# Optimization experiments

Hardware: AMD Instinct MI355X
Metric: run time of the kernel (lower is better)

Reference implementation:

```python
import jax, jax.numpy as jnp
import numpy as np

B, T, D, H, O = 256, 512, 128, 256, 128

def setup_inputs() -> dict:
    key = jax.random.key(0)
    ks = jax.random.split(key, 7)
    s = lambda k, shape, fan: jax.random.normal(k, shape, dtype=jnp.float32) / np.sqrt(fan)
    return {
        "x": jax.random.normal(ks[0], (B, T, D), dtype=jnp.float32),
        "W_hx_w": s(ks[1], (H, D), D),
        "W_hx_b": jnp.zeros((H,), jnp.float32),
        "W_hh_w": s(ks[2], (H, H), H),
        "W_hh_b": jnp.zeros((H,), jnp.float32),
        "W_ph_w": s(ks[3], (O, H), H),
        "W_ph_b": jnp.zeros((O,), jnp.float32),
    }

def reference(x, W_hx_w, W_hx_b, W_hh_w, W_hh_b, W_ph_w, W_ph_b):
    # Precompute the input projection for all timesteps in one batched GEMM.
    xW = jnp.einsum('btd,hd->bth', x, W_hx_w) + W_hx_b  # [B,T,H]
    h0 = jnp.zeros((x.shape[0], W_hh_w.shape[0]), x.dtype)

    def step(h, xw_t):
        h_new = jnp.tanh(xw_t + h @ W_hh_w.T + W_hh_b)
        return h_new, None

    h_T, _ = jax.lax.scan(step, h0, jnp.swapaxes(xW, 0, 1))  # scan over T
    out = h_T @ W_ph_w.T + W_ph_b  # [B,O]
    return out
```

## Files before the change

### kernel.cpp

```cpp
#include <hip/hip_runtime.h>


typedef _Float16 f16;
typedef _Float16 f16x2 __attribute__((ext_vector_type(2)));
typedef _Float16 f16x4 __attribute__((ext_vector_type(4)));
typedef _Float16 f16x8 __attribute__((ext_vector_type(8)));
typedef float f32x4 __attribute__((ext_vector_type(4)));

#define NB 256
#define NT 512
#define ND 128
#define NH 256
#define NO 128
#define R  16
#define TCH 8
#define NCH (NT / TCH)
#define STEP_F16 4096
#define WS_NEED ((size_t)16 * NT * STEP_F16 * 2)

__device__ __forceinline__ float fast_tanh(float z) {
  float e = __builtin_amdgcn_exp2f(z * 2.88539008177793f);
  float r = __builtin_amdgcn_rcpf(e + 1.0f);
  return __builtin_fmaf(-2.0f, r, 1.0f);
}

__device__ __forceinline__ f16x8 cvt8(const float* __restrict__ p) {
  f32x4 v0 = *(const f32x4*)p;
  f32x4 v1 = *(const f32x4*)(p + 4);
  f16x8 r;
  r[0] = (f16)v0.x; r[1] = (f16)v0.y; r[2] = (f16)v0.z; r[3] = (f16)v0.w;
  r[4] = (f16)v1.x; r[5] = (f16)v1.y; r[6] = (f16)v1.z; r[7] = (f16)v1.w;
  return r;
}

__global__ __launch_bounds__(256, 1)
void xw_gemm(const float* __restrict__ x,
             const float* __restrict__ Wx, const float* __restrict__ bx,
             const float* __restrict__ bh, f16* __restrict__ ws)
{
  const int wgb = blockIdx.x & 15;
  const int c   = blockIdx.x >> 4;
  const int tid = threadIdx.x;
  const int w   = tid >> 6;
  const int l15 = tid & 15;
  const int g   = (tid >> 4) & 3;

  __shared__ alignas(16) f16 xlds[TCH * R][ND];

  f16x8 fWx[4][4];
  f32x4 bias4[4];
  #pragma unroll
  for (int ct = 0; ct < 4; ++ct) {
    const int j = w * 64 + ct * 16 + l15;
    #pragma unroll
    for (int kt = 0; kt < 4; ++kt)
      fWx[ct][kt] = cvt8(Wx + (size_t)j * ND + kt * 32 + g * 8);
    const int j0 = w * 64 + ct * 16 + g * 4;
    #pragma unroll
    for (int rg = 0; rg < 4; ++rg)
      bias4[ct][rg] = bx[j0 + rg] + bh[j0 + rg];
  }

  const int srow = tid >> 4;
  const int sq   = tid & 15;
  const float* xc = x + ((size_t)(wgb * R + srow) * NT + (size_t)c * TCH) * ND;
  #pragma unroll
  for (int jj = 0; jj < 16; ++jj) {
    const int f = (sq + jj * 16) * 4;
    f32x4 v = *(const f32x4*)(xc + f);
    const int t = f >> 7;
    const int d = f & (ND - 1);
    const int m = t * R + srow;
    f16x4 h4;
    h4[0] = (f16)v.x; h4[1] = (f16)v.y; h4[2] = (f16)v.z; h4[3] = (f16)v.w;
    *(f16x4*)((char*)&xlds[m][0] + ((2 * d) ^ ((m & 7) << 4))) = h4;
  }
  __syncthreads();

  #pragma unroll
  for (int t = 0; t < TCH; ++t) {
    f16x8 b[4];
    #pragma unroll
    for (int kt = 0; kt < 4; ++kt) {
      const int m = t * R + l15;
      b[kt] = *(const f16x8*)((char*)&xlds[m][0] +
               ((kt * 64 + g * 16) ^ ((m & 7) << 4)));
    }
    f16* wsp = ws + ((size_t)(wgb * NT + c * TCH + t)) * STEP_F16
                  + w * 1024 + g * 64 + l15 * 4;
    #pragma unroll
    for (int ct = 0; ct < 4; ++ct) {
      f32x4 ac = bias4[ct];
      #pragma unroll
      for (int kt = 0; kt < 4; ++kt)
        ac = __builtin_amdgcn_mfma_f32_16x16x32_f16(fWx[ct][kt], b[kt], ac, 0, 0, 0);
      f16x4 p;
      p[0] = (f16)ac[0]; p[1] = (f16)ac[1]; p[2] = (f16)ac[2]; p[3] = (f16)ac[3];
      *(f16x4*)(wsp + ct * 256) = p;
    }
  }
}

#define DO_STEP(CUR, ACIN, ACOUT, XWPF, XWIN, TAU)                          \
  {                                                                         \
    f16x8 bfr[8];                                                           \
    _Pragma("unroll")                                                       \
    for (int kt = 0; kt < 8; ++kt)                                          \
      bfr[kt] = *(const f16x8*)((const char*)&hbuf[CUR][l15][0] +           \
                ((kt * 64 + g * 16) ^ ((l15 & 7) << 4)));                   \
    int pf = (TAU) + 2; pf = pf < NT ? pf : NT - 1;                         \
    _Pragma("unroll")                                                       \
    for (int ct = 0; ct < 2; ++ct)                                          \
      XWPF[ct] = *(const f16x4*)(wsg + (size_t)pf * STEP_F16 + ct * 256);   \
    _Pragma("unroll")                                                       \
    for (int ct = 0; ct < 2; ++ct) {                                        \
      _Pragma("unroll")                                                     \
      for (int kt = 0; kt < 8; ++kt)                                        \
        ACIN[ct] = __builtin_amdgcn_mfma_f32_16x16x32_f16(fWh[ct][kt],      \
                     bfr[kt], ACIN[ct], 0, 0, 0);                           \
    }                                                                       \
    _Pragma("unroll")                                                       \
    for (int ct = 0; ct < 2; ++ct) {                                        \
      f16x4 h4;                                                             \
      _Pragma("unroll")                                                     \
      for (int rg = 0; rg < 4; ++rg)                                        \
        h4[rg] = (f16)fast_tanh(ACIN[ct][rg]);                              \
      *(f16x4*)((char*)&hbuf[(CUR) ^ 1][l15][0] +                           \
                ((64 * w2 + 32 * ct + 8 * g) ^ ((l15 & 7) << 4))) = h4;     \
    }                                                                       \
    _Pragma("unroll")                                                       \
    for (int ct = 0; ct < 2; ++ct) {                                        \
      ACOUT[ct][0] = (float)XWIN[ct][0]; ACOUT[ct][1] = (float)XWIN[ct][1]; \
      ACOUT[ct][2] = (float)XWIN[ct][2]; ACOUT[ct][3] = (float)XWIN[ct][3]; \
    }                                                                       \
    asm volatile("s_waitcnt lgkmcnt(0)\n\ts_barrier" ::: "memory");         \
    __builtin_amdgcn_sched_barrier(0);                                      \
  }

__global__ __launch_bounds__(512, 2)
void rnn_scan(const f16* __restrict__ ws,
              const float* __restrict__ Wh,
              const float* __restrict__ Wp, const float* __restrict__ bp,
              float* __restrict__ out)
{
  const int wg  = blockIdx.x;
  const int tid = threadIdx.x;
  const int w2  = tid >> 6;
  const int l15 = tid & 15;
  const int g   = (tid >> 4) & 3;

  __shared__ alignas(16) f16 hbuf[2][R][NH];

  f16x8 fWh[2][8];
  #pragma unroll
  for (int ct = 0; ct < 2; ++ct) {
    const int j = w2 * 32 + ct * 16 + l15;
    #pragma unroll
    for (int kt = 0; kt < 8; ++kt)
      fWh[ct][kt] = cvt8(Wh + (size_t)j * NH + kt * 32 + g * 8);
  }

  {
    unsigned* hz = (unsigned*)&hbuf[0][0][0];
    #pragma unroll
    for (int k = 0; k < (2 * R * NH / 2) / 512; ++k) hz[tid + k * 512] = 0u;
  }

  const f16* wsg = ws + (size_t)wg * NT * STEP_F16
                 + (size_t)(w2 * 2) * 256 + g * 64 + l15 * 4;

  f16x4 xA[2], xB[2];
  #pragma unroll
  for (int ct = 0; ct < 2; ++ct) xA[ct] = *(const f16x4*)(wsg + 0 * STEP_F16 + ct * 256);
  #pragma unroll
  for (int ct = 0; ct < 2; ++ct) xB[ct] = *(const f16x4*)(wsg + 1 * STEP_F16 + ct * 256);

  f32x4 acA[2], acB[2];
  #pragma unroll
  for (int ct = 0; ct < 2; ++ct) {
    acA[ct][0] = (float)xA[ct][0]; acA[ct][1] = (float)xA[ct][1];
    acA[ct][2] = (float)xA[ct][2]; acA[ct][3] = (float)xA[ct][3];
  }
  __syncthreads();

  #pragma unroll 1
  for (int tau = 0; tau < NT; tau += 2) {
    DO_STEP(0, acA, acB, xA, xB, tau);
    DO_STEP(1, acB, acA, xB, xA, tau + 1);
  }

  f16x8 bh8[8];
  #pragma unroll
  for (int kt = 0; kt < 8; ++kt)
    bh8[kt] = *(const f16x8*)((const char*)&hbuf[0][l15][0] +
              ((kt * 64 + g * 16) ^ ((l15 & 7) << 4)));
  {
    const int j0 = w2 * 16 + g * 4;
    f32x4 ac = {bp[j0], bp[j0 + 1], bp[j0 + 2], bp[j0 + 3]};
    #pragma unroll
    for (int kt = 0; kt < 8; ++kt) {
      f16x8 afr = cvt8(Wp + (size_t)(w2 * 16 + l15) * NH + kt * 32 + g * 8);
      ac = __builtin_amdgcn_mfma_f32_16x16x32_f16(afr, bh8[kt], ac, 0, 0, 0);
    }
    #pragma unroll
    for (int rg = 0; rg < 4; ++rg)
      out[(size_t)(wg * R + l15) * NO + j0 + rg] = ac[rg];
  }
}

__global__ __launch_bounds__(256, 1)
void rnn_mfma(const float* __restrict__ x,
              const float* __restrict__ Wx, const float* __restrict__ bx,
              const float* __restrict__ Wh, const float* __restrict__ bh,
              const float* __restrict__ Wp, const float* __restrict__ bp,
              float* __restrict__ out)
{
  const int wg  = blockIdx.x;
  const int tid = threadIdx.x;
  const int w   = tid >> 6;
  const int l15 = tid & 15;
  const int g   = (tid >> 4) & 3;

  __shared__ alignas(16) f16 xlds[TCH * R][ND];
  __shared__ alignas(16) f16 hbuf[2][R][NH];

  f16x8 fWh[4][8];
  #pragma unroll
  for (int ct = 0; ct < 4; ++ct) {
    const int j = w * 64 + ct * 16 + l15;
    #pragma unroll
    for (int kt = 0; kt < 8; ++kt)
      fWh[ct][kt] = cvt8(Wh + (size_t)j * NH + kt * 32 + g * 8);
  }
  f16x8 fWx[4][4];
  #pragma unroll
  for (int ct = 0; ct < 4; ++ct) {
    const int j = w * 64 + ct * 16 + l15;
    #pragma unroll
    for (int kt = 0; kt < 4; ++kt)
      fWx[ct][kt] = cvt8(Wx + (size_t)j * ND + kt * 32 + g * 8);
  }
  float bias[4];
  #pragma unroll
  for (int ct = 0; ct < 4; ++ct) {
    const int j = w * 64 + ct * 16 + l15;
    bias[ct] = bx[j] + bh[j];
  }
  {
    unsigned* hz = (unsigned*)&hbuf[0][0][0];
    #pragma unroll
    for (int k = 0; k < (R * NH / 2) / 256; ++k) hz[tid + k * 256] = 0u;
  }
  __syncthreads();

  int cur = 0;
  f16x2 xwb[TCH][4][2];
  const int srow = tid >> 4;
  const int sq   = tid & 15;
  const float* xrow = x + (size_t)(wg * R + srow) * NT * ND;

  #pragma unroll 1
  for (int c = 0; c < NCH; ++c) {
    const float* xc = xrow + (size_t)c * TCH * ND;
    #pragma unroll
    for (int jj = 0; jj < 16; ++jj) {
      const int f = (sq + jj * 16) * 4;
      f32x4 v = *(const f32x4*)(xc + f);
      const int t = f >> 7;
      const int d = f & (ND - 1);
      const int m = t * R + srow;
      f16x4 h4;
      h4[0] = (f16)v.x; h4[1] = (f16)v.y; h4[2] = (f16)v.z; h4[3] = (f16)v.w;
      *(f16x4*)((char*)&xlds[m][0] + ((2 * d) ^ ((m & 7) << 4))) = h4;
    }
    __syncthreads();

    #pragma unroll
    for (int t = 0; t < TCH; ++t) {
      f16x8 a[4];
      #pragma unroll
      for (int kt = 0; kt < 4; ++kt) {
        const int m = t * R + l15;
        a[kt] = *(const f16x8*)((char*)&xlds[m][0] +
                 ((kt * 64 + g * 16) ^ ((m & 7) << 4)));
      }
      #pragma unroll
      for (int ct = 0; ct < 4; ++ct) {
        f32x4 ac = {bias[ct], bias[ct], bias[ct], bias[ct]};
        #pragma unroll
        for (int kt = 0; kt < 4; ++kt)
          ac = __builtin_amdgcn_mfma_f32_16x16x32_f16(a[kt], fWx[ct][kt], ac, 0, 0, 0);
        f16x2 p0; p0[0] = (f16)ac[0]; p0[1] = (f16)ac[1];
        f16x2 p1; p1[0] = (f16)ac[2]; p1[1] = (f16)ac[3];
        xwb[t][ct][0] = p0;
        xwb[t][ct][1] = p1;
      }
    }

    #pragma unroll
    for (int s = 0; s < TCH; ++s) {
      f16x8 a[8];
      #pragma unroll
      for (int kt = 0; kt < 8; ++kt) {
        const int m = l15;
        a[kt] = *(const f16x8*)((char*)&hbuf[cur][m][0] +
                 ((kt * 64 + g * 16) ^ ((m & 7) << 4)));
      }
      const int nxt = cur ^ 1;
      #pragma unroll
      for (int ct = 0; ct < 4; ++ct) {
        f32x4 ac  = {(float)xwb[s][ct][0][0], (float)xwb[s][ct][0][1],
                     (float)xwb[s][ct][1][0], (float)xwb[s][ct][1][1]};
        f32x4 ac2 = {0.f, 0.f, 0.f, 0.f};
        #pragma unroll
        for (int kt = 0; kt < 4; ++kt) {
          ac  = __builtin_amdgcn_mfma_f32_16x16x32_f16(a[2*kt],     fWh[ct][2*kt],     ac,  0, 0, 0);
          ac2 = __builtin_amdgcn_mfma_f32_16x16x32_f16(a[2*kt + 1], fWh[ct][2*kt + 1], ac2, 0, 0, 0);
        }
        #pragma unroll
        for (int rg = 0; rg < 4; ++rg) {
          const float th = fast_tanh(ac[rg] + ac2[rg]);
          const int row = g * 4 + rg;
          const int col = w * 64 + ct * 16 + l15;
          *(f16*)((char*)&hbuf[nxt][row][0] +
                  ((2 * col) ^ ((row & 7) << 4))) = (f16)th;
        }
      }
      cur = nxt;
      __syncthreads();
    }
  }

  f16x8 ah[8];
  #pragma unroll
  for (int kt = 0; kt < 8; ++kt) {
    const int m = l15;
    ah[kt] = *(const f16x8*)((char*)&hbuf[cur][m][0] +
             ((kt * 64 + g * 16) ^ ((m & 7) << 4)));
  }
  #pragma unroll
  for (int ct = 0; ct < 2; ++ct) {
    const int o = w * 32 + ct * 16 + l15;
    f32x4 ac = {bp[o], bp[o], bp[o], bp[o]};
    #pragma unroll
    for (int kt = 0; kt < 8; ++kt) {
      f16x8 bfr = cvt8(Wp + (size_t)o * NH + kt * 32 + g * 8);
      ac = __builtin_amdgcn_mfma_f32_16x16x32_f16(ah[kt], bfr, ac, 0, 0, 0);
    }
    #pragma unroll
    for (int rg = 0; rg < 4; ++rg) {
      const int row = g * 4 + rg;
      out[(size_t)(wg * R + row) * NO + o] = ac[rg];
    }
  }
}

extern "C" void kernel_launch(void* const* d_in, const int* in_sizes, int n_in,
                              void* d_out, int out_size, void* d_ws, size_t ws_size,
                              hipStream_t stream) {
  const float* x   = (const float*)d_in[0];
  const float* whx = (const float*)d_in[1];
  const float* bhx = (const float*)d_in[2];
  const float* whh = (const float*)d_in[3];
  const float* bhh = (const float*)d_in[4];
  const float* wph = (const float*)d_in[5];
  const float* bph = (const float*)d_in[6];
  float* out = (float*)d_out;

  if (ws_size >= WS_NEED) {
    f16* ws = (f16*)d_ws;
    xw_gemm<<<dim3(16 * NCH), dim3(256), 0, stream>>>(x, whx, bhx, bhh, ws);
    rnn_scan<<<dim3(16), dim3(512), 0, stream>>>(ws, whh, wph, bph, out);
  } else {
    rnn_mfma<<<dim3(NB / R), dim3(256), 0, stream>>>(x, whx, bhx, whh, bhh, wph, bph, out);
  }
}
```

Measured before the change: 338.8 us.

## Permute K layout of hidden state and weights; persist xW GEMM blocks over chunks

The scan's hidden-state LDS layout is changed to a rotated 16-byte-slot scheme. The K dimension of the recurrent and projection weight fragments is permuted to match, so each wave writes its two column tiles as one 8-half store instead of two 4-half stores. The input-projection GEMM now launches 256 blocks that each loop over four time chunks, which amortises the per-block conversion of Wx to fp16 and the bias setup. The rotated layout is meant to avoid LDS bank conflicts on the per-step critical path, but it relies on the weight K permutation being exactly consistent.

```diff
diff --git a/kernel.cpp b/kernel.cpp
--- a/kernel.cpp
+++ b/kernel.cpp
@@ -33,13 +33,24 @@
   return r;
 }
 
+__device__ __forceinline__ f16x8 cvt44(const float* __restrict__ p0,
+                                       const float* __restrict__ p1) {
+  f32x4 a = *(const f32x4*)p0;
+  f32x4 b = *(const f32x4*)p1;
+  f16x8 r;
+  r[0] = (f16)a.x; r[1] = (f16)a.y; r[2] = (f16)a.z; r[3] = (f16)a.w;
+  r[4] = (f16)b.x; r[5] = (f16)b.y; r[6] = (f16)b.z; r[7] = (f16)b.w;
+  return r;
+}
+
 __global__ __launch_bounds__(256, 1)
 void xw_gemm(const float* __restrict__ x,
              const float* __restrict__ Wx, const float* __restrict__ bx,
              const float* __restrict__ bh, f16* __restrict__ ws)
 {
-  const int wgb = blockIdx.x & 15;
-  const int c   = blockIdx.x >> 4;
+  const int bid = blockIdx.x;
+  const int wgb = bid & 15;
+  const int c0  = (bid >> 4) * 4;
   const int tid = threadIdx.x;
   const int w   = tid >> 6;
   const int l15 = tid & 15;
@@ -63,40 +74,47 @@
 
   const int srow = tid >> 4;
   const int sq   = tid & 15;
-  const float* xc = x + ((size_t)(wgb * R + srow) * NT + (size_t)c * TCH) * ND;
-  #pragma unroll
-  for (int jj = 0; jj < 16; ++jj) {
-    const int f = (sq + jj * 16) * 4;
-    f32x4 v = *(const f32x4*)(xc + f);
-    const int t = f >> 7;
-    const int d = f & (ND - 1);
-    const int m = t * R + srow;
-    f16x4 h4;
-    h4[0] = (f16)v.x; h4[1] = (f16)v.y; h4[2] = (f16)v.z; h4[3] = (f16)v.w;
-    *(f16x4*)((char*)&xlds[m][0] + ((2 * d) ^ ((m & 7) << 4))) = h4;
-  }
-  __syncthreads();
-
-  #pragma unroll
-  for (int t = 0; t < TCH; ++t) {
-    f16x8 b[4];
-    #pragma unroll
-    for (int kt = 0; kt < 4; ++kt) {
-      const int m = t * R + l15;
-      b[kt] = *(const f16x8*)((char*)&xlds[m][0] +
-               ((kt * 64 + g * 16) ^ ((m & 7) << 4)));
-    }
-    f16* wsp = ws + ((size_t)(wgb * NT + c * TCH + t)) * STEP_F16
-                  + w * 1024 + g * 64 + l15 * 4;
-    #pragma unroll
-    for (int ct = 0; ct < 4; ++ct) {
-      f32x4 ac = bias4[ct];
-      #pragma unroll
-      for (int kt = 0; kt < 4; ++kt)
-        ac = __builtin_amdgcn_mfma_f32_16x16x32_f16(fWx[ct][kt], b[kt], ac, 0, 0, 0);
-      f16x4 p;
-      p[0] = (f16)ac[0]; p[1] = (f16)ac[1]; p[2] = (f16)ac[2]; p[3] = (f16)ac[3];
-      *(f16x4*)(wsp + ct * 256) = p;
+
+  #pragma unroll 1
+  for (int it = 0; it < 4; ++it) {
+    const int c = c0 + it;
+    if (it) __syncthreads();
+
+    const float* xc = x + ((size_t)(wgb * R + srow) * NT + (size_t)c * TCH) * ND;
+    #pragma unroll
+    for (int jj = 0; jj < 16; ++jj) {
+      const int f = (sq + jj * 16) * 4;
+      f32x4 v = *(const f32x4*)(xc + f);
+      const int t = f >> 7;
+      const int d = f & (ND - 1);
+      const int m = t * R + srow;
+      f16x4 h4;
+      h4[0] = (f16)v.x; h4[1] = (f16)v.y; h4[2] = (f16)v.z; h4[3] = (f16)v.w;
+      *(f16x4*)((char*)&xlds[m][0] + ((2 * d) ^ ((m & 7) << 4))) = h4;
+    }
+    __syncthreads();
+
+    #pragma unroll
+    for (int t = 0; t < TCH; ++t) {
+      f16x8 b[4];
+      #pragma unroll
+      for (int kt = 0; kt < 4; ++kt) {
+        const int m = t * R + l15;
+        b[kt] = *(const f16x8*)((char*)&xlds[m][0] +
+                 ((kt * 64 + g * 16) ^ ((m & 7) << 4)));
+      }
+      f16* wsp = ws + ((size_t)(wgb * NT + c * TCH + t)) * STEP_F16
+                    + w * 1024 + g * 64 + l15 * 4;
+      #pragma unroll
+      for (int ct = 0; ct < 4; ++ct) {
+        f32x4 ac = bias4[ct];
+        #pragma unroll
+        for (int kt = 0; kt < 4; ++kt)
+          ac = __builtin_amdgcn_mfma_f32_16x16x32_f16(fWx[ct][kt], b[kt], ac, 0, 0, 0);
+        f16x4 p;
+        p[0] = (f16)ac[0]; p[1] = (f16)ac[1]; p[2] = (f16)ac[2]; p[3] = (f16)ac[3];
+        *(f16x4*)(wsp + ct * 256) = p;
+      }
     }
   }
 }
@@ -107,7 +125,7 @@
     _Pragma("unroll")                                                       \
     for (int kt = 0; kt < 8; ++kt)                                          \
       bfr[kt] = *(const f16x8*)((const char*)&hbuf[CUR][l15][0] +           \
-                ((kt * 64 + g * 16) ^ ((l15 & 7) << 4)));                   \
+                (((kt * 4 + g + l15) & 31) << 4));                          \
     int pf = (TAU) + 2; pf = pf < NT ? pf : NT - 1;                         \
     _Pragma("unroll")                                                       \
     for (int ct = 0; ct < 2; ++ct)                                          \
@@ -119,14 +137,15 @@
         ACIN[ct] = __builtin_amdgcn_mfma_f32_16x16x32_f16(fWh[ct][kt],      \
                      bfr[kt], ACIN[ct], 0, 0, 0);                           \
     }                                                                       \
-    _Pragma("unroll")                                                       \
-    for (int ct = 0; ct < 2; ++ct) {                                        \
-      f16x4 h4;                                                             \
+    {                                                                       \
+      f16x8 h8;                                                             \
       _Pragma("unroll")                                                     \
-      for (int rg = 0; rg < 4; ++rg)                                        \
-        h4[rg] = (f16)fast_tanh(ACIN[ct][rg]);                              \
-      *(f16x4*)((char*)&hbuf[(CUR) ^ 1][l15][0] +                           \
-                ((64 * w2 + 32 * ct + 8 * g) ^ ((l15 & 7) << 4))) = h4;     \
+      for (int ct = 0; ct < 2; ++ct)                                        \
+        _Pragma("unroll")                                                   \
+        for (int rg = 0; rg < 4; ++rg)                                      \
+          h8[ct * 4 + rg] = (f16)fast_tanh(ACIN[ct][rg]);                   \
+      *(f16x8*)((char*)&hbuf[(CUR) ^ 1][l15][0] +                           \
+                (((w2 * 4 + g + l15) & 31) << 4)) = h8;                     \
     }                                                                       \
     _Pragma("unroll")                                                       \
     for (int ct = 0; ct < 2; ++ct) {                                        \
@@ -157,7 +176,8 @@
     const int j = w2 * 32 + ct * 16 + l15;
     #pragma unroll
     for (int kt = 0; kt < 8; ++kt)
-      fWh[ct][kt] = cvt8(Wh + (size_t)j * NH + kt * 32 + g * 8);
+      fWh[ct][kt] = cvt44(Wh + (size_t)j * NH + kt * 32 + g * 4,
+                          Wh + (size_t)j * NH + kt * 32 + 16 + g * 4);
   }
 
   {
@@ -193,13 +213,14 @@
   #pragma unroll
   for (int kt = 0; kt < 8; ++kt)
     bh8[kt] = *(const f16x8*)((const char*)&hbuf[0][l15][0] +
-              ((kt * 64 + g * 16) ^ ((l15 & 7) << 4)));
+              (((kt * 4 + g + l15) & 31) << 4));
   {
     const int j0 = w2 * 16 + g * 4;
     f32x4 ac = {bp[j0], bp[j0 + 1], bp[j0 + 2], bp[j0 + 3]};
     #pragma unroll
     for (int kt = 0; kt < 8; ++kt) {
-      f16x8 afr = cvt8(Wp + (size_t)(w2 * 16 + l15) * NH + kt * 32 + g * 8);
+      const float* wrow = Wp + (size_t)(w2 * 16 + l15) * NH;
+      f16x8 afr = cvt44(wrow + kt * 32 + g * 4, wrow + kt * 32 + 16 + g * 4);
       ac = __builtin_amdgcn_mfma_f32_16x16x32_f16(afr, bh8[kt], ac, 0, 0, 0);
     }
     #pragma unroll
@@ -369,7 +390,7 @@
 
   if (ws_size >= WS_NEED) {
     f16* ws = (f16*)d_ws;
-    xw_gemm<<<dim3(16 * NCH), dim3(256), 0, stream>>>(x, whx, bhx, bhh, ws);
+    xw_gemm<<<dim3(256), dim3(256), 0, stream>>>(x, whx, bhx, bhh, ws);
     rnn_scan<<<dim3(16), dim3(512), 0, stream>>>(ws, whh, wph, bph, out);
   } else {
     rnn_mfma<<<dim3(NB / R), dim3(256), 0, stream>>>(x, whx, bhx, whh, bhh, wph, bph, out);
```

New measurement: 339.7 us. About the same (+0.3%).
